# Kernel tuning notes

Measured on AMD Instinct MI355X. Metric: run time of the kernel, lower is better.

## Reference

```python
import jax, jax.numpy as jnp
import numpy as np

B, T, N = 32, 720, 321
K = 25        # moving-average kernel_size (init kwarg)
DEC_LEV = 3   # wavelet decomposition level (init kwarg)
F = 16        # sym8 filter length
A = 0.85      # soft-threshold shrink factor from the source

# pywt sym8 decomposition low-pass filter
_DEC_LO = np.array([
    -0.0033824159510061256, -0.00054213233179114812, 0.031695087811492981,
    0.0076074873249176054, -0.14329423835080971, -0.061273359067658524,
    0.48135965125837221, 0.77718575170052351, 0.36444189483533893,
    -0.051945838107709037, -0.027219029917056003, 0.049137179673607506,
    0.0038087520138906151, -0.014952258337048231, -0.0003029205147213668,
    0.0018899503327594609], dtype=np.float32)
_DEC_HI = (((-1.0) ** (np.arange(F) + 1)) * _DEC_LO[::-1]).astype(np.float32)
DEC_LO = jnp.asarray(_DEC_LO)
DEC_HI = jnp.asarray(_DEC_HI)
REC_LO = DEC_LO[::-1]
REC_HI = DEC_HI[::-1]


def _dwt(a):
    # single-level DWT, pywt 'symmetric' extension, downsample odd phase
    ext = jnp.pad(a, (F - 1, F - 1), mode='symmetric')
    ca = jnp.convolve(ext, DEC_LO, mode='valid')[1::2]
    cd = jnp.convolve(ext, DEC_HI, mode='valid')[1::2]
    return ca, cd


def _idwt(ca, cd):
    # upsample (zeros in odd slots), full conv with reconstruction filters, trim F-2
    L = ca.shape[0]
    up_a = jnp.zeros(2 * L - 1, ca.dtype).at[::2].set(ca)
    up_d = jnp.zeros(2 * L - 1, cd.dtype).at[::2].set(cd)
    rec = jnp.convolve(up_a, REC_LO) + jnp.convolve(up_d, REC_HI)
    return rec[F - 2: rec.shape[0] - (F - 2)]


def _denoise(sig):
    # wavedec -> universal soft-threshold (shrunk by A) on all detail levels -> waverec
    L = sig.shape[0]
    a = sig
    details = []  # details[0] = finest level cD1
    for _ in range(DEC_LEV):
        a, d = _dwt(a)
        details.append(d)
    sigma = jnp.median(jnp.abs(details[0])) / 0.6745
    lam = sigma * jnp.sqrt(jnp.float32(2.0 * np.log(float(L))))
    details = [jnp.where(jnp.abs(d) >= lam,
                         jnp.sign(d) * (jnp.abs(d) - A * lam),
                         jnp.zeros_like(d)) for d in details]
    for d in reversed(details):
        if a.shape[0] == d.shape[0] + 1:  # static-shape pywt length fixup
            a = a[:-1]
        a = _idwt(a, d)
    return a


def _moving_avg(x):
    # replicate-pad (K-1)//2 on both ends of time axis, then AvgPool1d(K, stride=1)
    p = (K - 1) // 2
    xp = jnp.concatenate([jnp.repeat(x[:, :1], p, axis=1), x,
                          jnp.repeat(x[:, -1:], p, axis=1)], axis=1)
    s = jax.lax.reduce_window(xp, 0.0, jax.lax.add, (1, K, 1), (1, 1, 1), 'VALID')
    return s / K


def _forward(x):
    trend = _moving_avg(x)            # [B,T,N]
    res = x - trend
    # T is even so the odd-length branch of the original is never taken
    trend_nn = _denoise(trend.reshape(-1)).reshape(x.shape)
    res_nn = _denoise(res.reshape(-1)).reshape(x.shape)
    return trend - trend_nn, trend_nn, res - res_nn, res_nn


def setup_inputs() -> dict:
    key = jax.random.key(0)
    return {"x": jax.random.normal(key, (B, T, N), dtype=jnp.float32)}


def reference(x):
    return _forward(x)
```

## Files before the change

### kernel.cpp

```cpp
#include <hip/hip_runtime.h>
#include <math.h>

#define BB 32
#define TT 720
#define NNN 321
#define KK 25
#define PP 12
#define TCH 24

constexpr int L0 = BB * TT * NNN;
constexpr int L1 = (L0 + 15) / 2;
constexpr int L2 = (L1 + 15) / 2;
constexpr int L3 = (L2 + 15) / 2;
constexpr int L1P = L1 + 1;
constexpr int L2P = L2 + 1;
constexpr int L3P = L3 + 1;
constexpr unsigned KMED = (unsigned)((L1 - 1) / 2 + 1);
constexpr float AA = 0.85f;

constexpr int NH1B = 512;
constexpr int CH   = (L1 + NH1B - 1) / NH1B;
constexpr int CANDSZ = NH1B * CH;

#define NC3 1024
constexpr int LEN2T = 2 * NC3 + 32;
constexpr int LEN1T = 4 * NC3 + 80;
#define NF0 4096
constexpr int N1T = NF0 / 2 + 8;
constexpr int N2T = N1T / 2 + 7;
constexpr int NQ3 = (N2T + 1) / 2;

constexpr float DLO[16] = {
    -0.0033824159510061256f, -0.0005421323317911481f, 0.03169508781149298f,
    0.007607487324917605f,  -0.1432942383508097f,    -0.061273359067658524f,
    0.4813596512583722f,     0.7771857517005235f,     0.36444189483533895f,
    -0.05194583810770904f,  -0.027219029917056003f,   0.049137179673607506f,
    0.003808752013890615f,  -0.01495225833704823f,   -0.0003029205147213668f,
    0.0018899503327594609f };

__device__ void select_body(unsigned* hist, unsigned* prefix, unsigned* kArr,
                            float* lamArr, int nbins, int shift) {
    int t = threadIdx.x;
    int chunk = nbins >> 8;
    __shared__ unsigned wsum[4];
    for (int s = 0; s < 2; ++s) {
        unsigned loc[16];
        unsigned* hs = hist + s * 4096 + t * chunk;
        unsigned csum = 0;
        for (int j = 0; j < chunk; ++j) { loc[j] = atomicExch(&hs[j], 0u); csum += loc[j]; }
        unsigned v = csum;
        int lane = t & 63, wv = t >> 6;
#pragma unroll
        for (int off = 1; off < 64; off <<= 1) {
            unsigned u = (unsigned)__shfl_up((int)v, off, 64);
            if (lane >= off) v += u;
        }
        if (lane == 63) wsum[wv] = v;
        __syncthreads();
        unsigned base = 0;
        for (int w2 = 0; w2 < wv; ++w2) base += wsum[w2];
        unsigned incl = base + v, excl = incl - csum;
        unsigned k = kArr[s];
        if (excl < k && incl >= k) {
            unsigned run = excl;
            for (int j = 0; j < chunk; ++j) {
                if (run < k && run + loc[j] >= k) {
                    unsigned digit = (unsigned)(t * chunk + j);
                    unsigned npref = prefix[s] | (digit << shift);
                    prefix[s] = npref;
                    kArr[s] = k - run;
                    if (shift == 0) {
                        float med = __uint_as_float(npref);
                        lamArr[s] = (med / 0.6745f) * sqrtf(2.0f * logf((float)L0));
                    }
                    break;
                }
                run += loc[j];
            }
        }
        __syncthreads();
    }
}

__device__ bool i_am_last(unsigned* done, unsigned nBlocks) {
    __shared__ int amLast;
    __syncthreads();
    if (threadIdx.x == 0) {
        unsigned prev = atomicAdd(done, 1u);
        amLast = (prev == nBlocks - 1) ? 1 : 0;
    }
    __syncthreads();
    return amLast != 0;
}

__global__ void mavg_kernel(const float* __restrict__ x,
                            float* __restrict__ trend,
                            float* __restrict__ res,
                            unsigned* __restrict__ hist,
                            unsigned* __restrict__ prefix,
                            unsigned* __restrict__ kArr,
                            unsigned* __restrict__ done) {
    constexpr int NCH = TT / TCH;
    int gid = blockIdx.x * blockDim.x + threadIdx.x;
    if (gid < 8192) hist[gid] = 0;
    if (gid < 2) { prefix[gid] = 0; kArr[gid] = KMED; }
    if (gid < 3) done[gid] = 0;
    if (gid >= BB * NCH * NNN) return;
    int n    = gid % NNN;
    int rest = gid / NNN;
    int ch   = rest % NCH;
    int b    = rest / NCH;
    int t0   = ch * TCH;
    const float* xb = x + (size_t)b * TT * NNN + n;
    float sum = 0.f;
#pragma unroll
    for (int dt = -PP; dt <= PP; ++dt) {
        int tt = t0 + dt;
        tt = tt < 0 ? 0 : (tt >= TT ? TT - 1 : tt);
        sum += xb[(size_t)tt * NNN];
    }
    size_t base = (size_t)b * TT * NNN + (size_t)t0 * NNN + n;
    for (int i = 0; i < TCH; ++i) {
        int t = t0 + i;
        float tr = sum * (1.0f / (float)KK);
        size_t idx = base + (size_t)i * NNN;
        trend[idx] = tr;
        res[idx] = xb[(size_t)t * NNN] - tr;
        int tp = t + 1 + PP; if (tp > TT - 1) tp = TT - 1;
        int tm = t - PP;     if (tm < 0)      tm = 0;
        sum += xb[(size_t)tp * NNN] - xb[(size_t)tm * NNN];
    }
}

__global__ void dwt123_kernel(const float* __restrict__ trend,
                              const float* __restrict__ res,
                              float* __restrict__ cd1,
                              float* __restrict__ cd2,
                              float* __restrict__ ca3,
                              float* __restrict__ cd3,
                              unsigned* __restrict__ hist,
                              unsigned* __restrict__ prefix,
                              unsigned* __restrict__ kArr,
                              float* __restrict__ lamArr,
                              unsigned* __restrict__ done) {
    int s = blockIdx.y;
    int C0 = blockIdx.x * NC3;
    const float* a0 = s ? res : trend;
    __shared__ float s1[LEN1T];
    __shared__ float s2[LEN2T];
    unsigned* shst = (unsigned*)s2;

    for (int b = threadIdx.x; b < 2048; b += 256) shst[b] = 0;
    __syncthreads();

    int T0 = 2 * C0 - 14;
    int S1 = 4 * C0 - 42; if (S1 < 0) S1 = 0;
    int E1 = 2 * (T0 + LEN2T) + 2; if (E1 > L1) E1 = L1;
    int len1 = E1 - S1;
    float* pcd1 = cd1 + (size_t)s * L1P;

    int npair = (len1 + 1) / 2;
    for (int ip = threadIdx.x; ip < npair; ip += 256) {
        int i = 2 * ip;
        int o = S1 + i;
        float slo0, shi0, slo1, shi1;
        if (2 * o - 16 >= 0 && 2 * o + 3 < L0) {
            const float4* p4 = (const float4*)(a0 + 2 * o - 16);
            float4 qa = p4[0], qb = p4[1], qc = p4[2], qd = p4[3], qe = p4[4];
            float v[20] = { qa.x,qa.y,qa.z,qa.w, qb.x,qb.y,qb.z,qb.w,
                            qc.x,qc.y,qc.z,qc.w, qd.x,qd.y,qd.z,qd.w,
                            qe.x,qe.y,qe.z,qe.w };
            slo0 = shi0 = slo1 = shi1 = 0.f;
#pragma unroll
            for (int j = 0; j < 16; ++j) {
                float h = (j & 1) ? DLO[15 - j] : -DLO[15 - j];
                slo0 = fmaf(DLO[j], v[17 - j], slo0);
                shi0 = fmaf(h,      v[17 - j], shi0);
                slo1 = fmaf(DLO[j], v[19 - j], slo1);
                shi1 = fmaf(h,      v[19 - j], shi1);
            }
        } else {
            float acc[2][2];
#pragma unroll
            for (int q = 0; q < 2; ++q) {
                int oo = o + q;
                float slo = 0.f, shi = 0.f;
                int bidx = 2 * oo + 1;
#pragma unroll
                for (int j = 0; j < 16; ++j) {
                    int idx = bidx - j;
                    if (idx < 0) idx = -1 - idx;
                    if (idx >= L0) idx = 2 * L0 - 1 - idx;
                    float v = a0[idx];
                    slo = fmaf(DLO[j], v, slo);
                    float h = (j & 1) ? DLO[15 - j] : -DLO[15 - j];
                    shi = fmaf(h, v, shi);
                }
                acc[q][0] = slo; acc[q][1] = shi;
            }
            slo0 = acc[0][0]; shi0 = acc[0][1];
            slo1 = acc[1][0]; shi1 = acc[1][1];
        }
        s1[i] = slo0;
        if (i + 1 < len1) s1[i + 1] = slo1;
        if (o >= 4 * C0 && o < 4 * C0 + 4 * NC3) {
            unsigned u0 = __float_as_uint(fabsf(shi0));
            if (i + 1 < len1) {
                *(float2*)(pcd1 + o) = make_float2(shi0, shi1);
                unsigned u1 = __float_as_uint(fabsf(shi1));
                atomicAdd(&shst[u0 >> 21], 1u);
                atomicAdd(&shst[u1 >> 21], 1u);
            } else {
                pcd1[o] = shi0;
                atomicAdd(&shst[u0 >> 21], 1u);
            }
        }
    }
    __syncthreads();

    for (int b = threadIdx.x; b < 2048; b += 256) {
        unsigned c = shst[b];
        if (c) atomicAdd(&hist[s * 4096 + b], c);
    }
    __syncthreads();

    float* pcd2 = cd2 + (size_t)s * L2P;
    for (int ip = threadIdx.x; ip < LEN2T / 2; ip += 256) {
        int i0 = 2 * ip;
        int e0 = T0 + i0;
        int e1 = e0 + 1;
        if (2 * e0 - 14 >= 0 && 2 * e1 + 1 < L1 && e1 < L2) {
            const float2* wp2 = (const float2*)(s1 + (2 * e0 - 14 - S1));
            float w[18];
#pragma unroll
            for (int j = 0; j < 9; ++j) { float2 t2 = wp2[j]; w[2*j] = t2.x; w[2*j+1] = t2.y; }
            float slo0 = 0.f, shi0 = 0.f, slo1 = 0.f, shi1 = 0.f;
#pragma unroll
            for (int j = 0; j < 16; ++j) {
                float h = (j & 1) ? DLO[15 - j] : -DLO[15 - j];
                slo0 = fmaf(DLO[j], w[15 - j], slo0);
                shi0 = fmaf(h,      w[15 - j], shi0);
                slo1 = fmaf(DLO[j], w[17 - j], slo1);
                shi1 = fmaf(h,      w[17 - j], shi1);
            }
            s2[i0] = slo0; s2[i0 + 1] = slo1;
            if (e0 >= 2 * C0 && e0 < 2 * C0 + 2 * NC3)
                *(float2*)(pcd2 + e0) = make_float2(shi0, shi1);
        } else {
#pragma unroll
            for (int q = 0; q < 2; ++q) {
                int i = i0 + q;
                int e = T0 + i;
                if (e < 0 || e >= L2) continue;
                int base = 2 * e + 1;
                float slo = 0.f, shi = 0.f;
#pragma unroll
                for (int j = 0; j < 16; ++j) {
                    int idx = base - j;
                    if (idx < 0) idx = -1 - idx;
                    if (idx >= L1) idx = 2 * L1 - 1 - idx;
                    float v = s1[idx - S1];
                    slo = fmaf(DLO[j], v, slo);
                    float h = (j & 1) ? DLO[15 - j] : -DLO[15 - j];
                    shi = fmaf(h, v, shi);
                }
                s2[i] = slo;
                if (e >= 2 * C0 && e < 2 * C0 + 2 * NC3) pcd2[e] = shi;
            }
        }
    }
    __syncthreads();
    for (int i = threadIdx.x; i < LEN2T; i += 256) {
        int e = T0 + i;
        if (e < 0)        s2[i] = s2[(-1 - e) - T0];
        else if (e >= L2) s2[i] = s2[(2 * L2 - 1 - e) - T0];
    }
    __syncthreads();
    float* pca3 = ca3 + (size_t)s * L3P;
    float* pcd3 = cd3 + (size_t)s * L3P;
    for (int ip = threadIdx.x; ip < NC3 / 2; ip += 256) {
        int i0 = 2 * ip;
        int o0 = C0 + i0;
        if (o0 >= L3) break;
        const float2* wp2 = (const float2*)(s2 + i0 * 2);
        float w[18];
#pragma unroll
        for (int j = 0; j < 9; ++j) { float2 t2 = wp2[j]; w[2*j] = t2.x; w[2*j+1] = t2.y; }
        float slo0 = 0.f, shi0 = 0.f, slo1 = 0.f, shi1 = 0.f;
#pragma unroll
        for (int j = 0; j < 16; ++j) {
            float h = (j & 1) ? DLO[15 - j] : -DLO[15 - j];
            slo0 = fmaf(DLO[j], w[15 - j], slo0);
            shi0 = fmaf(h,      w[15 - j], shi0);
            slo1 = fmaf(DLO[j], w[17 - j], slo1);
            shi1 = fmaf(h,      w[17 - j], shi1);
        }
        if (o0 + 1 < L3) {
            *(float2*)(pca3 + o0) = make_float2(slo0, slo1);
            *(float2*)(pcd3 + o0) = make_float2(shi0, shi1);
        } else {
            pca3[o0] = slo0; pcd3[o0] = shi0;
        }
    }

    if (i_am_last(done + 0, gridDim.x * gridDim.y))
        select_body(hist, prefix, kArr, lamArr, 2048, 21);
}

__device__ __forceinline__ float sthr(float d, float lam, float alam) {
    float ad = fabsf(d);
    return (ad >= lam) ? copysignf(ad - alam, d) : 0.f;
}

__global__ void idwt_fused(const float* __restrict__ ca3,
                           const float* __restrict__ cd3,
                           const float* __restrict__ cd2,
                           const float* __restrict__ cd1,
                           const float* __restrict__ trend,
                           const float* __restrict__ res,
                           float* __restrict__ out,
                           const float* __restrict__ lamArr) {
    int s = blockIdx.y;
    int F0 = blockIdx.x * NF0;
    float lam = lamArr[s], alam = AA * lam;
    const float* pa3 = ca3 + (size_t)s * L3P;
    const float* pd3 = cd3 + (size_t)s * L3P;
    const float* pd2 = cd2 + (size_t)s * L2P;
    const float* pd1 = cd1 + (size_t)s * L1P;
    __shared__ float r2[N2T + 1];
    __shared__ float r1[N1T];
    int A1 = F0 >> 1, A2 = F0 >> 2, Q3 = F0 >> 3;
    for (int i = threadIdx.x; i < NQ3; i += 256) {
        int q3 = Q3 + i;
        float a0 = 0.f, a1 = 0.f;
#pragma unroll
        for (int p = 0; p < 8; ++p) {
            int idx = q3 + p; if (idx > L3 - 1) idx = L3 - 1;
            float a = pa3[idx];
            float d = sthr(pd3[idx], lam, alam);
            a0 = fmaf(a, DLO[2 * p + 1], a0);
            a0 = fmaf(d, DLO[14 - 2 * p], a0);
            a1 = fmaf(a, DLO[2 * p], a1);
            a1 = fmaf(d, -DLO[15 - 2 * p], a1);
        }
        r2[2 * i] = a0; r2[2 * i + 1] = a1;
    }
    __syncthreads();
    for (int i = threadIdx.x; i < N1T / 2; i += 256) {
        int q2 = A2 + i;
        float a0 = 0.f, a1 = 0.f;
#pragma unroll
        for (int p = 0; p < 8; ++p) {
            float a = r2[i + p];
            int idx = q2 + p; if (idx > L2 - 1) idx = L2 - 1;
            float d = sthr(pd2[idx], lam, alam);
            a0 = fmaf(a, DLO[2 * p + 1], a0);
            a0 = fmaf(d, DLO[14 - 2 * p], a0);
            a1 = fmaf(a, DLO[2 * p], a1);
            a1 = fmaf(d, -DLO[15 - 2 * p], a1);
        }
        r1[2 * i] = a0; r1[2 * i + 1] = a1;
    }
    __syncthreads();
    const float* orig = s ? res : trend;
    float* o_diff = out + (size_t)(2 * s) * L0;
    float* o_nn   = out + (size_t)(2 * s + 1) * L0;
    for (int i = threadIdx.x; i < NF0 / 4; i += 256) {
        int ii = 2 * i;
        int q1 = A1 + ii;
        int r0 = 2 * q1;
        if (r0 >= L0) break;
        float d[9];
        if (q1 + 9 <= L1) {
            const float2* pp = (const float2*)(pd1 + q1);
            float2 e0 = pp[0], e1 = pp[1], e2 = pp[2], e3 = pp[3];
            d[0] = sthr(e0.x, lam, alam); d[1] = sthr(e0.y, lam, alam);
            d[2] = sthr(e1.x, lam, alam); d[3] = sthr(e1.y, lam, alam);
            d[4] = sthr(e2.x, lam, alam); d[5] = sthr(e2.y, lam, alam);
            d[6] = sthr(e3.x, lam, alam); d[7] = sthr(e3.y, lam, alam);
            d[8] = sthr(pd1[q1 + 8], lam, alam);
        } else {
#pragma unroll
            for (int p = 0; p < 9; ++p) {
                int idx = q1 + p; if (idx > L1 - 1) idx = L1 - 1;
                d[p] = sthr(pd1[idx], lam, alam);
            }
        }
        float a0 = 0.f, a1 = 0.f, b0 = 0.f, b1 = 0.f;
#pragma unroll
        for (int p = 0; p < 8; ++p) {
            float a  = r1[ii + p];
            float ab = r1[ii + 1 + p];
            a0 = fmaf(a,      DLO[2 * p + 1], a0);
            a0 = fmaf(d[p],   DLO[14 - 2 * p], a0);
            a1 = fmaf(a,      DLO[2 * p], a1);
            a1 = fmaf(d[p],  -DLO[15 - 2 * p], a1);
            b0 = fmaf(ab,     DLO[2 * p + 1], b0);
            b0 = fmaf(d[p+1], DLO[14 - 2 * p], b0);
            b1 = fmaf(ab,     DLO[2 * p], b1);
            b1 = fmaf(d[p+1],-DLO[15 - 2 * p], b1);
        }
        float4 o4 = *(const float4*)(orig + r0);
        float4 nn; nn.x = a0; nn.y = a1; nn.z = b0; nn.w = b1;
        float4 df; df.x = o4.x - a0; df.y = o4.y - a1; df.z = o4.z - b0; df.w = o4.w - b1;
        *(float4*)(o_nn + r0)   = nn;
        *(float4*)(o_diff + r0) = df;
    }
}

__global__ void hist1_kernel(const float* __restrict__ d,
                             unsigned* __restrict__ hist,
                             unsigned* __restrict__ prefix,
                             unsigned* __restrict__ cand,
                             unsigned* __restrict__ bcnt,
                             unsigned* __restrict__ kArr,
                             float* __restrict__ lamArr,
                             unsigned* __restrict__ done) {
    int s = blockIdx.y;
    int blk = blockIdx.x;
    const float* ds = d + (size_t)s * L1P;
    unsigned* cs = cand + (size_t)s * CANDSZ + (size_t)blk * CH;
    __shared__ unsigned sh[4096];
    __shared__ unsigned slocal;
    for (int b = threadIdx.x; b < 4096; b += 256) sh[b] = 0;
    if (threadIdx.x == 0) slocal = 0;
    __syncthreads();
    unsigned pref = prefix[s] >> 21;
    int i0 = blk * CH;
    int i1 = i0 + CH; if (i1 > L1) i1 = L1;
    for (int i = i0 + threadIdx.x; i < i1; i += 256) {
        unsigned u = __float_as_uint(fabsf(ds[i]));
        if ((u >> 21) == pref) {
            atomicAdd(&sh[(u >> 9) & 0xFFFu], 1u);
            unsigned pos = atomicAdd(&slocal, 1u);
            cs[pos] = u;
        }
    }
    __syncthreads();
    if (threadIdx.x == 0) bcnt[s * NH1B + blk] = slocal;
    for (int b = threadIdx.x; b < 4096; b += 256) {
        unsigned c = sh[b];
        if (c) atomicAdd(&hist[s * 4096 + b], c);
    }
    if (i_am_last(done + 1, gridDim.x * gridDim.y))
        select_body(hist, prefix, kArr, lamArr, 4096, 9);
}

__global__ void hist2_kernel(const unsigned* __restrict__ cand,
                             unsigned* __restrict__ hist,
                             unsigned* __restrict__ prefix,
                             const unsigned* __restrict__ bcnt,
                             unsigned* __restrict__ kArr,
                             float* __restrict__ lamArr,
                             unsigned* __restrict__ done) {
    int s = blockIdx.y;
    int blk = blockIdx.x;
    const unsigned* cs = cand + (size_t)s * CANDSZ + (size_t)blk * CH;
    __shared__ unsigned sh[512];
    sh[threadIdx.x] = 0; sh[threadIdx.x + 256] = 0;
    __syncthreads();
    unsigned pref = prefix[s] >> 9;
    unsigned n = bcnt[s * NH1B + blk];
    for (unsigned i = threadIdx.x; i < n; i += 256) {
        unsigned u = cs[i];
        if ((u >> 9) == pref) atomicAdd(&sh[u & 0x1FFu], 1u);
    }
    __syncthreads();
    for (int b = threadIdx.x; b < 512; b += 256) {
        unsigned c = sh[b];
        if (c) atomicAdd(&hist[s * 4096 + b], c);
    }
    if (i_am_last(done + 2, gridDim.x * gridDim.y))
        select_body(hist, prefix, kArr, lamArr, 512, 0);
}

extern "C" void kernel_launch(void* const* d_in, const int* in_sizes, int n_in,
                              void* d_out, int out_size, void* d_ws, size_t ws_size,
                              hipStream_t stream) {
    const float* x = (const float*)d_in[0];
    float* out = (float*)d_out;
    float* w = (float*)d_ws;

    float* trend = w;
    float* res   = w + (size_t)L0;
    float* cd1   = w + 2 * (size_t)L0;
    float* cd2   = cd1 + 2 * (size_t)L1P;
    float* ca3   = cd2 + 2 * (size_t)L2P;
    float* cd3   = ca3 + 2 * (size_t)L3P;
    unsigned* cand   = (unsigned*)(cd3 + 2 * (size_t)L3P);
    unsigned* hist   = cand + 2 * (size_t)CANDSZ;
    unsigned* prefix = hist + 8192;
    unsigned* kArr   = prefix + 2;
    float*    lamArr = (float*)(kArr + 2);
    unsigned* bcnt   = (unsigned*)(lamArr + 2);
    unsigned* done   = bcnt + 2 * NH1B;

    dim3 b256(256);

    {
        int nthreads = BB * (TT / TCH) * NNN;
        mavg_kernel<<<(nthreads + 255) / 256, b256, 0, stream>>>(
            x, trend, res, hist, prefix, kArr, done);
    }
    dwt123_kernel<<<dim3((L3 + NC3 - 1) / NC3, 2), b256, 0, stream>>>(
        trend, res, cd1, cd2, ca3, cd3, hist, prefix, kArr, lamArr, done);
    hist1_kernel<<<dim3(NH1B, 2), b256, 0, stream>>>(
        cd1, hist, prefix, cand, bcnt, kArr, lamArr, done);
    hist2_kernel<<<dim3(NH1B, 2), b256, 0, stream>>>(
        cand, hist, prefix, bcnt, kArr, lamArr, done);
    idwt_fused<<<dim3((L0 + NF0 - 1) / NF0, 2), b256, 0, stream>>>(
        ca3, cd3, cd2, cd1, trend, res, out, lamArr);
}
```

Baseline: 295.6 us.

## Vectorize moving average, histogram scan and IDWT output with wider loads

The moving-average kernel now gives each thread four adjacent channels using float4 loads and stores, with a scalar path for the last channel. The histogram candidate scan reads cd1 as float4. The final IDWT stage produces eight outputs per thread instead of four. Separately, the select step clears the histogram with 64-bit atomic exchanges, and the level-1 histogram merges identical-bin increments into one atomic. Because the channel count of 321 is not a multiple of four, the moving-average float4 accesses are unaligned, which relies on hardware unaligned-access support and may split memory transactions.

```diff
diff --git a/kernel.cpp b/kernel.cpp
--- a/kernel.cpp
+++ b/kernel.cpp
@@ -19,7 +19,7 @@
 constexpr float AA = 0.85f;
 
 constexpr int NH1B = 512;
-constexpr int CH   = (L1 + NH1B - 1) / NH1B;
+constexpr int CH   = 7224;
 constexpr int CANDSZ = NH1B * CH;
 
 #define NC3 1024
@@ -38,6 +38,9 @@
     0.003808752013890615f,  -0.01495225833704823f,   -0.0003029205147213668f,
     0.0018899503327594609f };
 
+__device__ __forceinline__ float4 ld4(const float* p) { return *(const float4*)p; }
+__device__ __forceinline__ void st4(float* p, float4 v) { *(float4*)p = v; }
+
 __device__ void select_body(unsigned* hist, unsigned* prefix, unsigned* kArr,
                             float* lamArr, int nbins, int shift) {
     int t = threadIdx.x;
@@ -45,9 +48,14 @@
     __shared__ unsigned wsum[4];
     for (int s = 0; s < 2; ++s) {
         unsigned loc[16];
-        unsigned* hs = hist + s * 4096 + t * chunk;
+        unsigned long long* hs64 = (unsigned long long*)(hist + s * 4096 + t * chunk);
         unsigned csum = 0;
-        for (int j = 0; j < chunk; ++j) { loc[j] = atomicExch(&hs[j], 0u); csum += loc[j]; }
+        for (int j = 0; j < chunk / 2; ++j) {
+            unsigned long long v64 = atomicExch(&hs64[j], 0ULL);
+            loc[2 * j]     = (unsigned)v64;
+            loc[2 * j + 1] = (unsigned)(v64 >> 32);
+            csum += loc[2 * j] + loc[2 * j + 1];
+        }
         unsigned v = csum;
         int lane = t & 63, wv = t >> 6;
 #pragma unroll
@@ -101,34 +109,69 @@
                             unsigned* __restrict__ kArr,
                             unsigned* __restrict__ done) {
     constexpr int NCH = TT / TCH;
+    constexpr int NG  = 81;
     int gid = blockIdx.x * blockDim.x + threadIdx.x;
     if (gid < 8192) hist[gid] = 0;
     if (gid < 2) { prefix[gid] = 0; kArr[gid] = KMED; }
     if (gid < 3) done[gid] = 0;
-    if (gid >= BB * NCH * NNN) return;
-    int n    = gid % NNN;
-    int rest = gid / NNN;
+    if (gid >= BB * NCH * NG) return;
+    int g    = gid % NG;
+    int rest = gid / NG;
     int ch   = rest % NCH;
     int b    = rest / NCH;
     int t0   = ch * TCH;
-    const float* xb = x + (size_t)b * TT * NNN + n;
-    float sum = 0.f;
-#pragma unroll
-    for (int dt = -PP; dt <= PP; ++dt) {
-        int tt = t0 + dt;
-        tt = tt < 0 ? 0 : (tt >= TT ? TT - 1 : tt);
-        sum += xb[(size_t)tt * NNN];
-    }
-    size_t base = (size_t)b * TT * NNN + (size_t)t0 * NNN + n;
-    for (int i = 0; i < TCH; ++i) {
-        int t = t0 + i;
-        float tr = sum * (1.0f / (float)KK);
-        size_t idx = base + (size_t)i * NNN;
-        trend[idx] = tr;
-        res[idx] = xb[(size_t)t * NNN] - tr;
-        int tp = t + 1 + PP; if (tp > TT - 1) tp = TT - 1;
-        int tm = t - PP;     if (tm < 0)      tm = 0;
-        sum += xb[(size_t)tp * NNN] - xb[(size_t)tm * NNN];
+    const float* xb = x + (size_t)b * TT * NNN;
+    size_t base = (size_t)b * TT * NNN + (size_t)t0 * NNN;
+    if (g < 80) {
+        int n = 4 * g;
+        const float* xc = xb + n;
+        float4 sum; sum.x = sum.y = sum.z = sum.w = 0.f;
+#pragma unroll
+        for (int dt = -PP; dt <= PP; ++dt) {
+            int tt = t0 + dt;
+            tt = tt < 0 ? 0 : (tt >= TT ? TT - 1 : tt);
+            float4 v = ld4(xc + (size_t)tt * NNN);
+            sum.x += v.x; sum.y += v.y; sum.z += v.z; sum.w += v.w;
+        }
+        for (int i = 0; i < TCH; ++i) {
+            int t = t0 + i;
+            float4 tr; tr.x = sum.x * (1.0f / (float)KK);
+            tr.y = sum.y * (1.0f / (float)KK);
+            tr.z = sum.z * (1.0f / (float)KK);
+            tr.w = sum.w * (1.0f / (float)KK);
+            size_t idx = base + (size_t)i * NNN + n;
+            st4(trend + idx, tr);
+            float4 c = ld4(xc + (size_t)t * NNN);
+            float4 rr; rr.x = c.x - tr.x; rr.y = c.y - tr.y;
+            rr.z = c.z - tr.z; rr.w = c.w - tr.w;
+            st4(res + idx, rr);
+            int tp = t + 1 + PP; if (tp > TT - 1) tp = TT - 1;
+            int tm = t - PP;     if (tm < 0)      tm = 0;
+            float4 vp = ld4(xc + (size_t)tp * NNN);
+            float4 vm = ld4(xc + (size_t)tm * NNN);
+            sum.x += vp.x - vm.x; sum.y += vp.y - vm.y;
+            sum.z += vp.z - vm.z; sum.w += vp.w - vm.w;
+        }
+    } else {
+        int n = 320;
+        const float* xc = xb + n;
+        float sum = 0.f;
+#pragma unroll
+        for (int dt = -PP; dt <= PP; ++dt) {
+            int tt = t0 + dt;
+            tt = tt < 0 ? 0 : (tt >= TT ? TT - 1 : tt);
+            sum += xc[(size_t)tt * NNN];
+        }
+        for (int i = 0; i < TCH; ++i) {
+            int t = t0 + i;
+            float tr = sum * (1.0f / (float)KK);
+            size_t idx = base + (size_t)i * NNN + n;
+            trend[idx] = tr;
+            res[idx] = xc[(size_t)t * NNN] - tr;
+            int tp = t + 1 + PP; if (tp > TT - 1) tp = TT - 1;
+            int tm = t - PP;     if (tm < 0)      tm = 0;
+            sum += xc[(size_t)tp * NNN] - xc[(size_t)tm * NNN];
+        }
     }
 }
 
@@ -208,8 +251,9 @@
             if (i + 1 < len1) {
                 *(float2*)(pcd1 + o) = make_float2(shi0, shi1);
                 unsigned u1 = __float_as_uint(fabsf(shi1));
-                atomicAdd(&shst[u0 >> 21], 1u);
-                atomicAdd(&shst[u1 >> 21], 1u);
+                unsigned b0 = u0 >> 21, b1 = u1 >> 21;
+                if (b0 == b1) atomicAdd(&shst[b0], 2u);
+                else { atomicAdd(&shst[b0], 1u); atomicAdd(&shst[b1], 1u); }
             } else {
                 pcd1[o] = shi0;
                 atomicAdd(&shst[u0 >> 21], 1u);
@@ -365,46 +409,54 @@
     const float* orig = s ? res : trend;
     float* o_diff = out + (size_t)(2 * s) * L0;
     float* o_nn   = out + (size_t)(2 * s + 1) * L0;
-    for (int i = threadIdx.x; i < NF0 / 4; i += 256) {
-        int ii = 2 * i;
+    for (int i = threadIdx.x; i < NF0 / 8; i += 256) {
+        int ii = 4 * i;
         int q1 = A1 + ii;
         int r0 = 2 * q1;
         if (r0 >= L0) break;
-        float d[9];
-        if (q1 + 9 <= L1) {
-            const float2* pp = (const float2*)(pd1 + q1);
-            float2 e0 = pp[0], e1 = pp[1], e2 = pp[2], e3 = pp[3];
+        float d[11];
+        if (q1 + 12 <= L1) {
+            const float4* pp = (const float4*)(pd1 + q1);
+            float4 e0 = pp[0], e1 = pp[1], e2 = pp[2];
             d[0] = sthr(e0.x, lam, alam); d[1] = sthr(e0.y, lam, alam);
-            d[2] = sthr(e1.x, lam, alam); d[3] = sthr(e1.y, lam, alam);
-            d[4] = sthr(e2.x, lam, alam); d[5] = sthr(e2.y, lam, alam);
-            d[6] = sthr(e3.x, lam, alam); d[7] = sthr(e3.y, lam, alam);
-            d[8] = sthr(pd1[q1 + 8], lam, alam);
+            d[2] = sthr(e0.z, lam, alam); d[3] = sthr(e0.w, lam, alam);
+            d[4] = sthr(e1.x, lam, alam); d[5] = sthr(e1.y, lam, alam);
+            d[6] = sthr(e1.z, lam, alam); d[7] = sthr(e1.w, lam, alam);
+            d[8] = sthr(e2.x, lam, alam); d[9] = sthr(e2.y, lam, alam);
+            d[10] = sthr(e2.z, lam, alam);
         } else {
 #pragma unroll
-            for (int p = 0; p < 9; ++p) {
+            for (int p = 0; p < 11; ++p) {
                 int idx = q1 + p; if (idx > L1 - 1) idx = L1 - 1;
                 d[p] = sthr(pd1[idx], lam, alam);
             }
         }
-        float a0 = 0.f, a1 = 0.f, b0 = 0.f, b1 = 0.f;
+        float acc0[4] = {0.f, 0.f, 0.f, 0.f};
+        float acc1[4] = {0.f, 0.f, 0.f, 0.f};
 #pragma unroll
         for (int p = 0; p < 8; ++p) {
-            float a  = r1[ii + p];
-            float ab = r1[ii + 1 + p];
-            a0 = fmaf(a,      DLO[2 * p + 1], a0);
-            a0 = fmaf(d[p],   DLO[14 - 2 * p], a0);
-            a1 = fmaf(a,      DLO[2 * p], a1);
-            a1 = fmaf(d[p],  -DLO[15 - 2 * p], a1);
-            b0 = fmaf(ab,     DLO[2 * p + 1], b0);
-            b0 = fmaf(d[p+1], DLO[14 - 2 * p], b0);
-            b1 = fmaf(ab,     DLO[2 * p], b1);
-            b1 = fmaf(d[p+1],-DLO[15 - 2 * p], b1);
-        }
-        float4 o4 = *(const float4*)(orig + r0);
-        float4 nn; nn.x = a0; nn.y = a1; nn.z = b0; nn.w = b1;
-        float4 df; df.x = o4.x - a0; df.y = o4.y - a1; df.z = o4.z - b0; df.w = o4.w - b1;
-        *(float4*)(o_nn + r0)   = nn;
-        *(float4*)(o_diff + r0) = df;
+#pragma unroll
+            for (int j = 0; j < 4; ++j) {
+                float a  = r1[ii + j + p];
+                float dd = d[j + p];
+                acc0[j] = fmaf(a,  DLO[2 * p + 1],  acc0[j]);
+                acc0[j] = fmaf(dd, DLO[14 - 2 * p], acc0[j]);
+                acc1[j] = fmaf(a,  DLO[2 * p],      acc1[j]);
+                acc1[j] = fmaf(dd, -DLO[15 - 2 * p], acc1[j]);
+            }
+        }
+        float4 o4a = *(const float4*)(orig + r0);
+        float4 o4b = *(const float4*)(orig + r0 + 4);
+        float4 nna; nna.x = acc0[0]; nna.y = acc1[0]; nna.z = acc0[1]; nna.w = acc1[1];
+        float4 nnb; nnb.x = acc0[2]; nnb.y = acc1[2]; nnb.z = acc0[3]; nnb.w = acc1[3];
+        float4 dfa; dfa.x = o4a.x - acc0[0]; dfa.y = o4a.y - acc1[0];
+        dfa.z = o4a.z - acc0[1]; dfa.w = o4a.w - acc1[1];
+        float4 dfb; dfb.x = o4b.x - acc0[2]; dfb.y = o4b.y - acc1[2];
+        dfb.z = o4b.z - acc0[3]; dfb.w = o4b.w - acc1[3];
+        *(float4*)(o_nn + r0)       = nna;
+        *(float4*)(o_nn + r0 + 4)   = nnb;
+        *(float4*)(o_diff + r0)     = dfa;
+        *(float4*)(o_diff + r0 + 4) = dfb;
     }
 }
 
@@ -428,12 +480,23 @@
     unsigned pref = prefix[s] >> 21;
     int i0 = blk * CH;
     int i1 = i0 + CH; if (i1 > L1) i1 = L1;
-    for (int i = i0 + threadIdx.x; i < i1; i += 256) {
-        unsigned u = __float_as_uint(fabsf(ds[i]));
-        if ((u >> 21) == pref) {
-            atomicAdd(&sh[(u >> 9) & 0xFFFu], 1u);
-            unsigned pos = atomicAdd(&slocal, 1u);
-            cs[pos] = u;
+    for (int i = i0 + 4 * (int)threadIdx.x; i < i1; i += 1024) {
+        if (i + 4 <= i1) {
+            float4 v = *(const float4*)(ds + i);
+            unsigned u;
+            u = __float_as_uint(fabsf(v.x));
+            if ((u >> 21) == pref) { atomicAdd(&sh[(u >> 9) & 0xFFFu], 1u); cs[atomicAdd(&slocal, 1u)] = u; }
+            u = __float_as_uint(fabsf(v.y));
+            if ((u >> 21) == pref) { atomicAdd(&sh[(u >> 9) & 0xFFFu], 1u); cs[atomicAdd(&slocal, 1u)] = u; }
+            u = __float_as_uint(fabsf(v.z));
+            if ((u >> 21) == pref) { atomicAdd(&sh[(u >> 9) & 0xFFFu], 1u); cs[atomicAdd(&slocal, 1u)] = u; }
+            u = __float_as_uint(fabsf(v.w));
+            if ((u >> 21) == pref) { atomicAdd(&sh[(u >> 9) & 0xFFFu], 1u); cs[atomicAdd(&slocal, 1u)] = u; }
+        } else {
+            for (int k = i; k < i1; ++k) {
+                unsigned u = __float_as_uint(fabsf(ds[k]));
+                if ((u >> 21) == pref) { atomicAdd(&sh[(u >> 9) & 0xFFFu], 1u); cs[atomicAdd(&slocal, 1u)] = u; }
+            }
         }
     }
     __syncthreads();
@@ -498,7 +561,7 @@
     dim3 b256(256);
 
     {
-        int nthreads = BB * (TT / TCH) * NNN;
+        int nthreads = BB * (TT / TCH) * 81;
         mavg_kernel<<<(nthreads + 255) / 256, b256, 0, stream>>>(
             x, trend, res, hist, prefix, kArr, done);
     }
```

New measurement: 297.0 us. Within noise of the previous version (+0.5%).
